# Optimization experiments

Hardware: AMD Instinct MI355X
Metric: run time of the kernel (lower is better)

The kernel has to match this reference:

```python
import jax, jax.numpy as jnp
import numpy as np

B, T, H, V, N_AT, KC, MAX_NB = 512, 64, 512, 780, 40, 4, 8
NMSG = B * T + 1  # message table size; slot 0 = zero padding vector


def setup_inputs() -> dict:
    key = jax.random.key(0)
    ks = jax.random.split(key, 24)
    s = 0.02
    f32 = jnp.float32
    w = lambda k, shp: jax.random.normal(k, shp, f32) * s
    inp = {}
    inp["node_rep"] = jax.random.normal(ks[0], (B, N_AT, H), f32)
    inp["clique_idx"] = jax.random.randint(ks[1], (B, T, KC), 0, N_AT)
    inp["root_clique_idx"] = jax.random.randint(ks[2], (B, KC), 0, N_AT)
    inp["nei_h_idx"] = jax.random.randint(ks[3], (B, T, MAX_NB), 0, NMSG)
    inp["nei_o_idx"] = jax.random.randint(ks[4], (B, T, MAX_NB), 0, NMSG)
    inp["root_nei_idx"] = jax.random.randint(ks[5], (B, MAX_NB), 0, NMSG)
    inp["direction"] = jax.random.randint(ks[6], (B, T), 0, 2)
    inp["pred_target"] = jax.random.randint(ks[7], (B, T), 0, V)
    inp["W_z_w"] = w(ks[8], (2 * H, H)); inp["W_z_b"] = jnp.zeros((H,), f32)
    inp["W_r_w"] = w(ks[9], (H, H));     inp["W_r_b"] = jnp.zeros((H,), f32)
    inp["U_r_w"] = w(ks[10], (H, H))  # no bias in torch U_r
    inp["W_h_w"] = w(ks[11], (2 * H, H)); inp["W_h_b"] = jnp.zeros((H,), f32)
    inp["W_w"] = w(ks[12], (H, H));     inp["W_b"] = jnp.zeros((H,), f32)
    inp["U_w"] = w(ks[13], (2 * H, H)); inp["U_b"] = jnp.zeros((H,), f32)
    inp["W_o_w"] = w(ks[14], (H, V));   inp["W_o_b"] = jnp.zeros((V,), f32)
    inp["U_s_w"] = w(ks[15], (H, 1));   inp["U_s_b"] = jnp.zeros((1,), f32)
    return inp


def _gru(x, h_nei, W_z_w, W_z_b, W_r_w, W_r_b, U_r_w, W_h_w, W_h_b):
    # x: [B,H]; h_nei: [B,MAX_NB,H]  (tree-GRU from the torch GRU() helper)
    sum_h = h_nei.sum(axis=1)
    z = jax.nn.sigmoid(jnp.concatenate([x, sum_h], axis=1) @ W_z_w + W_z_b)
    r = jax.nn.sigmoid((x @ W_r_w + W_r_b)[:, None, :] + h_nei @ U_r_w)
    sum_g = (r * h_nei).sum(axis=1)
    pre_h = jnp.tanh(jnp.concatenate([x, sum_g], axis=1) @ W_h_w + W_h_b)
    return (1.0 - z) * sum_h + z * pre_h


def reference(node_rep, clique_idx, root_clique_idx, nei_h_idx, nei_o_idx,
              root_nei_idx, direction, pred_target,
              W_z_w, W_z_b, W_r_w, W_r_b, U_r_w, W_h_w, W_h_b,
              W_w, W_b, U_w, U_b, W_o_w, W_o_b, U_s_w, U_s_b):
    dt = node_rep.dtype
    b_ar = jnp.arange(B)
    # x features: sum of node_rep over clique atom indices (torch index_select+sum)
    x_all = node_rep[b_ar[:, None, None], clique_idx].sum(axis=2)      # [B,T,H]
    root_x = node_rep[b_ar[:, None], root_clique_idx].sum(axis=1)      # [B,H]
    msg_ids = b_ar[:, None] * T + jnp.arange(T)[None, :] + 1           # [B,T]
    table0 = jnp.zeros((NMSG, H), dt)                                  # h dict -> flat table

    def step(table, xs):
        x_t, h_idx, o_idx, mid = xs
        h_nei = table[h_idx]                      # [B,MAX_NB,H] gather (excl. parent, pre-padded)
        new_h = _gru(x_t, h_nei, W_z_w, W_z_b, W_r_w, W_r_b, U_r_w, W_h_w, W_h_b)
        o = table[o_idx].sum(axis=1)              # [B,H] all-neighbor sum for stop head
        table = table.at[mid].set(new_h)          # scatter message back (h[x,y] = new_h)
        return table, (new_h, o)

    xs = (x_all.transpose(1, 0, 2), nei_h_idx.transpose(1, 0, 2),
          nei_o_idx.transpose(1, 0, 2), msg_ids.T)
    table, (new_h_all, o_all) = jax.lax.scan(step, table0, xs)
    new_h_all = new_h_all.transpose(1, 0, 2).reshape(B * T, H)         # [BT,H]
    o_all = o_all.transpose(1, 0, 2)                                   # [B,T,H]

    # stop head: all steps + final root step (target 0)
    stop_h = jnp.concatenate([x_all, o_all], axis=2).reshape(B * T, 2 * H)
    root_o = table[root_nei_idx].sum(axis=1)
    root_stop = jnp.concatenate([root_x, root_o], axis=1)
    stop_hiddens = jnp.concatenate([stop_h, root_stop], axis=0)        # [BT+B,2H]
    stop_targets = jnp.concatenate([direction.reshape(-1).astype(dt), jnp.zeros((B,), dt)])
    stop_scores = (jax.nn.relu(stop_hiddens @ U_w + U_b) @ U_s_w + U_s_b)[:, 0]
    # BCEWithLogits, sum reduction, / len(mol_batch)
    stop_loss = jnp.sum(jax.nn.softplus(stop_scores) - stop_scores * stop_targets) / B
    stop_acc = jnp.mean(((stop_scores >= 0).astype(dt) == stop_targets).astype(dt))

    # pred head on new_h where direction == 1
    pred_scores = jax.nn.relu(new_h_all @ W_w + W_b) @ W_o_w + W_o_b   # [BT,V]
    logp = jax.nn.log_softmax(pred_scores, axis=-1)
    tgt = pred_target.reshape(-1)
    ce = -jnp.take_along_axis(logp, tgt[:, None], axis=1)[:, 0]
    pmask = (direction.reshape(-1) == 1).astype(dt)
    pred_loss = jnp.sum(ce * pmask) / B                                # CE sum / len(mol_batch)
    preds = jnp.argmax(pred_scores, axis=1)
    pred_acc = jnp.sum((preds == tgt).astype(dt) * pmask) / jnp.sum(pmask)
    return (pred_loss, stop_loss, pred_acc, stop_acc)
```

## Files before the change

### kernel.cpp

```cpp
#include <hip/hip_runtime.h>
#include <math.h>

constexpr int B    = 512;
constexpr int T    = 64;
constexpr int H    = 512;
constexpr int V    = 780;
constexpr int N_AT = 40;
constexpr int KC   = 4;
constexpr int NB   = 8;
constexpr int BT   = B * T;
constexpr int NMSG = BT + 1;

template<int ASRC, int NSEG, int EPI>
__device__ __forceinline__ void gemm_core(
    float* smem, int bx, int by,
    const float* __restrict__ A1, const float* __restrict__ A2, int lda,
    const float* __restrict__ W, const float* __restrict__ bias,
    float* __restrict__ C, int ldc,
    const int* __restrict__ gidx, int gt, const float* __restrict__ table,
    const float* __restrict__ node_rep, const int* __restrict__ cliq,
    const float* __restrict__ o_all,
    const int* __restrict__ rci, const int* __restrict__ rni,
    const float* __restrict__ Ez, const float* __restrict__ Esh,
    const float* __restrict__ Usw, float* __restrict__ partial)
{
    float* As = smem;
    float* Ws = smem + 32 * 68;
    const int tid  = threadIdx.x;
    const int row0 = bx * 64;
    const int col0 = by * 64;
    const int tm   = tid >> 4;
    const int tn   = tid & 15;

    float acc[4][4] = {};

    const int ar0 = tid >> 5;
    const int ac  = tid & 31;
    const int wk0 = tid >> 6;
    const int wc  = tid & 63;

    for (int seg = 0; seg < NSEG; ++seg) {
        const float* Aseg = seg ? A2 : A1;
        const float* Wseg = W + (size_t)seg * H * H;
        for (int k0 = 0; k0 < H; k0 += 32) {
#pragma unroll
            for (int it = 0; it < 8; ++it) {
                const int r    = ar0 + it * 8;
                const int grow = row0 + r;
                float v;
                if (ASRC == 0) {
                    v = Aseg[(size_t)grow * lda + k0 + ac];
                } else if (ASRC == 1) {
                    const int gi = gidx[((grow >> 3) * T + gt) * NB + (grow & 7)];
                    v = table[(size_t)gi * H + k0 + ac];
                } else if (ASRC == 2) {
                    const int* ci = cliq + (size_t)grow * KC;
                    const int  b  = grow >> 6;
                    v = 0.f;
#pragma unroll
                    for (int j = 0; j < KC; ++j)
                        v += node_rep[((size_t)b * N_AT + ci[j]) * H + k0 + ac];
                } else {
                    if (grow < BT) {
                        if (seg == 0) {
                            const int* ci = cliq + (size_t)grow * KC;
                            const int  b  = grow >> 6;
                            v = 0.f;
#pragma unroll
                            for (int j = 0; j < KC; ++j)
                                v += node_rep[((size_t)b * N_AT + ci[j]) * H + k0 + ac];
                        } else {
                            v = o_all[(size_t)grow * H + k0 + ac];
                        }
                    } else {
                        const int b = grow - BT;
                        v = 0.f;
                        if (seg == 0) {
#pragma unroll
                            for (int j = 0; j < KC; ++j)
                                v += node_rep[((size_t)b * N_AT + rci[b * KC + j]) * H + k0 + ac];
                        } else {
#pragma unroll
                            for (int n = 0; n < NB; ++n)
                                v += table[(size_t)rni[b * NB + n] * H + k0 + ac];
                        }
                    }
                }
                As[(size_t)ac * 68 + r] = v;
                const int kk = wk0 + it * 4;
                Ws[(size_t)kk * 68 + wc] = Wseg[(size_t)(k0 + kk) * H + col0 + wc];
            }
            __syncthreads();
#pragma unroll
            for (int kk = 0; kk < 32; ++kk) {
                float a[4], w[4];
                *(float4*)a = *(const float4*)&As[kk * 68 + tm * 4];
                *(float4*)w = *(const float4*)&Ws[kk * 68 + tn * 4];
#pragma unroll
                for (int i = 0; i < 4; ++i)
#pragma unroll
                    for (int j = 0; j < 4; ++j)
                        acc[i][j] = fmaf(a[i], w[j], acc[i][j]);
            }
            __syncthreads();
        }
    }

    if (EPI == 4) {
        float* sred = smem + 2 * 32 * 68;
#pragma unroll
        for (int i = 0; i < 4; ++i) {
            float s = 0.f;
#pragma unroll
            for (int j = 0; j < 4; ++j) {
                const int ccol = col0 + tn * 4 + j;
                float val = acc[i][j] + bias[ccol];
                val = fmaxf(val, 0.f);
                s += val * Usw[ccol];
            }
            sred[(size_t)(tm * 4 + i) * 17 + tn] = s;
        }
        __syncthreads();
        if (tid < 64) {
            float s = 0.f;
#pragma unroll
            for (int t2 = 0; t2 < 16; ++t2) s += sred[(size_t)tid * 17 + t2];
            partial[(size_t)(row0 + tid) * 8 + by] = s;
        }
    } else {
#pragma unroll
        for (int i = 0; i < 4; ++i) {
            const int r = row0 + tm * 4 + i;
            float out[4];
#pragma unroll
            for (int j = 0; j < 4; ++j) {
                const int ccol = col0 + tn * 4 + j;
                float val = acc[i][j] + (bias ? bias[ccol] : 0.f);
                if (EPI == 1) {
                    val = 1.f / (1.f + expf(-val));
                } else if (EPI == 2) {
                    const float ph = tanhf(val);
                    const float zz = Ez[(size_t)r * H + ccol];
                    const float sh = Esh[(size_t)r * H + ccol];
                    val = (1.f - zz) * sh + zz * ph;
                } else if (EPI == 3) {
                    val = fmaxf(val, 0.f);
                }
                out[j] = val;
            }
            *(float4*)&C[(size_t)r * ldc + col0 + tn * 4] = *(float4*)out;
        }
    }
}

constexpr size_t SM_GEMM = (size_t)(2 * 32 * 68) * 4;
constexpr size_t SM_STOP = (size_t)(2 * 32 * 68 + 64 * 17) * 4;

template<int ASRC, int NSEG, int EPI>
__global__ __launch_bounds__(256)
void gemm_g(const float* __restrict__ A1, const float* __restrict__ A2, int lda,
            const float* __restrict__ W, const float* __restrict__ bias,
            float* __restrict__ C, int ldc,
            const int* __restrict__ gidx, int gt, const float* __restrict__ table,
            const float* __restrict__ node_rep, const int* __restrict__ cliq,
            const float* __restrict__ o_all,
            const int* __restrict__ rci, const int* __restrict__ rni,
            const float* __restrict__ Ez, const float* __restrict__ Esh,
            const float* __restrict__ Usw, float* __restrict__ partial)
{
    extern __shared__ float smem[];
    gemm_core<ASRC, NSEG, EPI>(smem, blockIdx.x, blockIdx.y, A1, A2, lda, W, bias,
                               C, ldc, gidx, gt, table, node_rep, cliq, o_all,
                               rci, rni, Ez, Esh, Usw, partial);
}

__global__ __launch_bounds__(256)
void step1_kernel(const int* __restrict__ nei_h, int t, const float* __restrict__ table,
                  const float* __restrict__ Urw, float* __restrict__ hU,
                  const float* __restrict__ xs, const float* __restrict__ Wzw,
                  const float* __restrict__ Wzb, float* __restrict__ zb)
{
    extern __shared__ float smem[];
    if (blockIdx.x < 64) {
        gemm_core<1, 1, 0>(smem, blockIdx.x, blockIdx.y, nullptr, nullptr, 0,
                           Urw, nullptr, hU, H, nei_h, t, table,
                           nullptr, nullptr, nullptr, nullptr, nullptr,
                           nullptr, nullptr, nullptr, nullptr);
    } else {
        gemm_core<0, 2, 1>(smem, blockIdx.x - 64, blockIdx.y, xs, xs + H, 2 * H,
                           Wzw, Wzb, zb, H, nullptr, 0, nullptr,
                           nullptr, nullptr, nullptr, nullptr, nullptr,
                           nullptr, nullptr, nullptr, nullptr);
    }
}

__global__ __launch_bounds__(256)
void pre2_kernel(const float* __restrict__ node_rep, const int* __restrict__ clique_idx,
                 const int* __restrict__ nei_h, const int* __restrict__ nei_o,
                 const float* __restrict__ table,
                 float* __restrict__ xs, float* __restrict__ hs, float* __restrict__ ss,
                 float* __restrict__ sumh, float* __restrict__ oDst, int oStride, int t)
{
    const int i = blockIdx.x * 256 + threadIdx.x;
    const int b = i >> 9, h = i & 511;
    const int* ci = clique_idx + ((size_t)b * T + t) * KC;
    float x = 0.f;
#pragma unroll
    for (int k = 0; k < KC; ++k)
        x += node_rep[((size_t)b * N_AT + ci[k]) * H + h];
    const int* hi = nei_h + ((size_t)b * T + t) * NB;
    const int* oi = nei_o + ((size_t)b * T + t) * NB;
    float sh = 0.f, so = 0.f;
#pragma unroll
    for (int n = 0; n < NB; ++n) {
        sh += table[(size_t)hi[n] * H + h];
        so += table[(size_t)oi[n] * H + h];
    }
    xs[(size_t)b * 1024 + h]       = x;
    xs[(size_t)b * 1024 + 512 + h] = sh;
    hs[(size_t)b * 1024 + h]       = x;
    ss[(size_t)b * 1024 + h]       = x;
    sumh[i] = sh;
    oDst[(size_t)b * oStride + h] = so;
}

__global__ __launch_bounds__(256)
void rsum2_kernel(const float* __restrict__ xrP, int xrStride,
                  const float* __restrict__ hU, const float* __restrict__ table,
                  const int* __restrict__ nei_h, float* __restrict__ hs, int t)
{
    const int i = blockIdx.x * 256 + threadIdx.x;
    const int b = i >> 9, h = i & 511;
    const int* hi = nei_h + ((size_t)b * T + t) * NB;
    const float xrv = xrP[(size_t)b * xrStride + h];
    float s = 0.f;
#pragma unroll
    for (int n = 0; n < NB; ++n) {
        const float hu = hU[((size_t)b * NB + n) * H + h];
        const float r  = 1.f / (1.f + expf(-(xrv + hu)));
        s += r * table[(size_t)hi[n] * H + h];
    }
    hs[(size_t)b * 1024 + 512 + h] = s;
}

__global__ __launch_bounds__(256)
void rootpre_kernel(const float* __restrict__ node_rep, const int* __restrict__ rci,
                    const int* __restrict__ rni, const float* __restrict__ table,
                    float* __restrict__ ss)
{
    const int i = blockIdx.x * 256 + threadIdx.x;
    const int b = i >> 9, h = i & 511;
    float x = 0.f;
#pragma unroll
    for (int k = 0; k < KC; ++k)
        x += node_rep[((size_t)b * N_AT + rci[b * KC + k]) * H + h];
    float so = 0.f;
#pragma unroll
    for (int n = 0; n < NB; ++n)
        so += table[(size_t)rni[b * NB + n] * H + h];
    ss[(size_t)b * 1024 + h]       = x;
    ss[(size_t)b * 1024 + 512 + h] = so;
}

__global__ __launch_bounds__(64)
void stopdot_kernel(const float* __restrict__ s1, const float* __restrict__ Usw,
                    const float* __restrict__ Usb,
                    float* __restrict__ out, int outStride, int outBase)
{
    const int b = blockIdx.x;
    const int lane = threadIdx.x;
    const float* row = s1 + (size_t)b * H;
    float s = 0.f;
    for (int h = lane; h < H; h += 64) s += row[h] * Usw[h];
#pragma unroll
    for (int off = 32; off; off >>= 1) s += __shfl_down(s, off);
    if (lane == 0) out[outBase + b * outStride] = s + Usb[0];
}

__global__ __launch_bounds__(256)
void stoploss_kernel(const float* __restrict__ scores, const int* __restrict__ direction,
                     float* __restrict__ accum)
{
    const int i = blockIdx.x * 256 + threadIdx.x;
    float loss = 0.f, acc = 0.f;
    if (i < BT + B) {
        const float s   = scores[i];
        const float tgt = (i < BT) ? (float)direction[i] : 0.f;
        loss = fmaxf(s, 0.f) - s * tgt + log1pf(expf(-fabsf(s)));
        const float p = (s >= 0.f) ? 1.f : 0.f;
        acc = (p == tgt) ? 1.f : 0.f;
    }
#pragma unroll
    for (int off = 32; off; off >>= 1) {
        loss += __shfl_down(loss, off);
        acc  += __shfl_down(acc, off);
    }
    if ((threadIdx.x & 63) == 0) {
        atomicAdd(&accum[3], loss);
        atomicAdd(&accum[4], acc);
    }
}

__global__ __launch_bounds__(256)
void stopfin_kernel(const float* __restrict__ partial, const float* __restrict__ Usb,
                    const int* __restrict__ direction, float* __restrict__ accum)
{
    const int i = blockIdx.x * 256 + threadIdx.x;
    float loss = 0.f, acc = 0.f;
    {
        float s = Usb[0];
#pragma unroll
        for (int cb = 0; cb < 8; ++cb) s += partial[(size_t)i * 8 + cb];
        const float tgt = (i < BT) ? (float)direction[i] : 0.f;
        loss = fmaxf(s, 0.f) - s * tgt + log1pf(expf(-fabsf(s)));
        const float p = (s >= 0.f) ? 1.f : 0.f;
        acc = (p == tgt) ? 1.f : 0.f;
    }
#pragma unroll
    for (int off = 32; off; off >>= 1) {
        loss += __shfl_down(loss, off);
        acc  += __shfl_down(acc, off);
    }
    if ((threadIdx.x & 63) == 0) {
        atomicAdd(&accum[3], loss);
        atomicAdd(&accum[4], acc);
    }
}

__global__ __launch_bounds__(256)
void ce_kernel(const float* __restrict__ s1_all, const float* __restrict__ Wo,
               const float* __restrict__ Wob, const int* __restrict__ direction,
               const int* __restrict__ ptgt, float* __restrict__ accum)
{
    __shared__ float s1T[512 * 34];
    __shared__ float Ws[32 * 68];
    __shared__ float blk[3];
    const int tid  = threadIdx.x;
    const int row0 = blockIdx.x * 32;

    for (int idx = tid; idx < 32 * 512; idx += 256) {
        const int r = idx >> 9, k = idx & 511;
        s1T[(size_t)k * 34 + r] = s1_all[(size_t)(row0 + r) * H + k];
    }
    if (tid < 3) blk[tid] = 0.f;
    __syncthreads();

    const int tm = tid >> 4, tn = tid & 15;
    const int tgt0 = ptgt[row0 + tm * 2];
    const int tgt1 = ptgt[row0 + tm * 2 + 1];
    float m0 = -1e30f, m1 = -1e30f, ss0 = 0.f, ss1 = 0.f, st0 = 0.f, st1 = 0.f;
    float bv0 = -1e30f, bv1 = -1e30f;
    int   bj0 = 0, bj1 = 0;

    for (int ct = 0; ct < 13; ++ct) {
        const int col0 = ct * 64;
        float acc[2][4] = {};
        for (int k0 = 0; k0 < 512; k0 += 32) {
#pragma unroll
            for (int it = 0; it < 8; ++it) {
                const int idx = tid + it * 256;
                const int kk = idx >> 6, cc = idx & 63;
                const int col = col0 + cc;
                Ws[(size_t)kk * 68 + cc] = (col < V) ? Wo[(size_t)(k0 + kk) * V + col] : 0.f;
            }
            __syncthreads();
#pragma unroll
            for (int kk = 0; kk < 32; ++kk) {
                const float a0 = s1T[(size_t)(k0 + kk) * 34 + tm * 2];
                const float a1 = s1T[(size_t)(k0 + kk) * 34 + tm * 2 + 1];
                float w[4];
                *(float4*)w = *(const float4*)&Ws[kk * 68 + tn * 4];
#pragma unroll
                for (int j = 0; j < 4; ++j) {
                    acc[0][j] = fmaf(a0, w[j], acc[0][j]);
                    acc[1][j] = fmaf(a1, w[j], acc[1][j]);
                }
            }
            __syncthreads();
        }
#pragma unroll
        for (int j = 0; j < 4; ++j) {
            const int col = col0 + tn * 4 + j;
// ... 76 lines not shown
    for (int j = 0; j < 16; ++j) {
        const int c = tx + j * 32;
        float acc = Wb[c];
        for (int k = 0; k < H; ++k) acc += hs[r][k] * Ww[(size_t)k * H + c];
        s1s[r][c] = fmaxf(acc, 0.f);
    }
    __syncthreads();
    const int row = row0 + r;
    const int tgt = ptgt[row];
    float m = -1e30f, ssum = 0.f, stgt = 0.f;
    float bestv = -1e30f; int bestj = 0;
    for (int v = tx; v < V; v += 32) {
        float sc = Wob[v];
        const float* wcol = Wo + v;
        for (int k = 0; k < H; ++k) sc += s1s[r][k] * wcol[(size_t)k * V];
        if (sc > m) { ssum = ssum * expf(m - sc) + 1.f; m = sc; }
        else        { ssum += expf(sc - m); }
        if (sc > bestv) { bestv = sc; bestj = v; }
        if (v == tgt) stgt = sc;
    }
#pragma unroll
    for (int off = 1; off < 32; off <<= 1) {
        const float om = __shfl_xor(m, off);
        const float os = __shfl_xor(ssum, off);
        const float nm = fmaxf(m, om);
        ssum = ssum * expf(m - nm) + os * expf(om - nm);
        m = nm;
        const float obv = __shfl_xor(bestv, off);
        const int   obj = __shfl_xor(bestj, off);
        if (obv > bestv || (obv == bestv && obj < bestj)) { bestv = obv; bestj = obj; }
        stgt += __shfl_xor(stgt, off);
    }
    if (tx == 0) {
        const float ce   = (m + logf(ssum)) - stgt;
        const float mask = (direction[row] == 1) ? 1.f : 0.f;
        const float corr = (bestj == tgt) ? 1.f : 0.f;
        atomicAdd(&accum[0], ce * mask);
        atomicAdd(&accum[1], mask);
        atomicAdd(&accum[2], corr * mask);
    }
}

__global__ void finalize_kernel(const float* __restrict__ accum, float* __restrict__ out)
{
    if (threadIdx.x == 0) {
        out[0] = accum[0] / (float)B;
        out[1] = accum[3] / (float)B;
        out[2] = accum[2] / accum[1];
        out[3] = accum[4] / (float)(BT + B);
    }
}

extern "C" void kernel_launch(void* const* d_in, const int* in_sizes, int n_in,
                              void* d_out, int out_size, void* d_ws, size_t ws_size,
                              hipStream_t stream)
{
    (void)in_sizes; (void)n_in; (void)out_size;

    const float* node_rep        = (const float*)d_in[0];
    const int*   clique_idx      = (const int*)d_in[1];
    const int*   root_clique_idx = (const int*)d_in[2];
    const int*   nei_h_idx       = (const int*)d_in[3];
    const int*   nei_o_idx       = (const int*)d_in[4];
    const int*   root_nei_idx    = (const int*)d_in[5];
    const int*   direction       = (const int*)d_in[6];
    const int*   pred_target     = (const int*)d_in[7];
    const float* W_z_w = (const float*)d_in[8];
    const float* W_z_b = (const float*)d_in[9];
    const float* W_r_w = (const float*)d_in[10];
    const float* W_r_b = (const float*)d_in[11];
    const float* U_r_w = (const float*)d_in[12];
    const float* W_h_w = (const float*)d_in[13];
    const float* W_h_b = (const float*)d_in[14];
    const float* W_w   = (const float*)d_in[15];
    const float* W_b   = (const float*)d_in[16];
    const float* U_w   = (const float*)d_in[17];
    const float* U_b   = (const float*)d_in[18];
    const float* W_o_w = (const float*)d_in[19];
    const float* W_o_b = (const float*)d_in[20];
    const float* U_s_w = (const float*)d_in[21];
    const float* U_s_b = (const float*)d_in[22];

    float* ws = (float*)d_ws;
    size_t off = 0;
    auto alloc = [&](size_t n) { float* p = ws + off; off += n; return p; };

    float* table  = alloc((size_t)NMSG * H);
    float* hU     = alloc((size_t)B * NB * H);
    float* xs     = alloc((size_t)B * 2 * H);
    float* hs     = alloc((size_t)B * 2 * H);
    float* ss     = alloc((size_t)B * 2 * H);
    float* sumh   = alloc((size_t)B * H);
    float* zb     = alloc((size_t)B * H);
    float* xr     = alloc((size_t)B * H);
    float* stop_scores = alloc(BT + B);
    float* accum  = alloc(8);

    const size_t availF = ws_size / sizeof(float);
    float *s1_all = nullptr, *o_all = nullptr, *partial = nullptr, *xr_all = nullptr;
    if (off + (size_t)BT * H <= availF)                 s1_all = alloc((size_t)BT * H);
    if (off + (size_t)BT * H + (size_t)(BT + B) * 8 <= availF) {
        o_all   = alloc((size_t)BT * H);
        partial = alloc((size_t)(BT + B) * 8);
    }
    if (off + (size_t)BT * H <= availF)                 xr_all = alloc((size_t)BT * H);

    hipMemsetAsync(table, 0, (size_t)NMSG * H * sizeof(float), stream);
    hipMemsetAsync(accum, 0, 8 * sizeof(float), stream);

    const int  BH_blocks = (B * H) / 256;
    const dim3 gSmall(8, 8);
    const dim3 gStep(72, 8);

    if (xr_all) {
        gemm_g<2, 1, 0><<<dim3(BT / 64, 8), 256, SM_GEMM, stream>>>(
            nullptr, nullptr, 0, W_r_w, W_r_b, xr_all, H,
            nullptr, 0, nullptr, node_rep, clique_idx,
            nullptr, nullptr, nullptr, nullptr, nullptr, nullptr, nullptr);
    }

    for (int t = 0; t < T; ++t) {
        float* oDst    = o_all ? (o_all + (size_t)t * H) : (ss + H);
        const int oStr = o_all ? (T * H) : (2 * H);
        pre2_kernel<<<BH_blocks, 256, 0, stream>>>(node_rep, clique_idx, nei_h_idx,
                                                   nei_o_idx, table, xs, hs, ss,
                                                   sumh, oDst, oStr, t);
        step1_kernel<<<gStep, 256, SM_GEMM, stream>>>(nei_h_idx, t, table, U_r_w, hU,
                                                      xs, W_z_w, W_z_b, zb);
        if (!xr_all) {
            gemm_g<0, 1, 0><<<gSmall, 256, SM_GEMM, stream>>>(
                xs, nullptr, 2 * H, W_r_w, W_r_b, xr, H,
                nullptr, 0, nullptr, nullptr, nullptr,
                nullptr, nullptr, nullptr, nullptr, nullptr, nullptr, nullptr);
        }
        const float* xrP   = xr_all ? (xr_all + (size_t)t * H) : xr;
        const int    xrStr = xr_all ? (T * H) : H;
        rsum2_kernel<<<BH_blocks, 256, 0, stream>>>(xrP, xrStr, hU, table,
                                                    nei_h_idx, hs, t);
        gemm_g<0, 2, 2><<<gSmall, 256, SM_GEMM, stream>>>(
            hs, hs + H, 2 * H, W_h_w, W_h_b, table + (size_t)(t + 1) * H, T * H,
            nullptr, 0, nullptr, nullptr, nullptr,
            nullptr, nullptr, nullptr, zb, sumh, nullptr, nullptr);
        if (!o_all) {
            gemm_g<0, 2, 3><<<gSmall, 256, SM_GEMM, stream>>>(
                ss, ss + H, 2 * H, U_w, U_b, zb, H,
                nullptr, 0, nullptr, nullptr, nullptr,
                nullptr, nullptr, nullptr, nullptr, nullptr, nullptr, nullptr);
            stopdot_kernel<<<B, 64, 0, stream>>>(zb, U_s_w, U_s_b, stop_scores, T, t);
        }
    }

    if (o_all) {
        gemm_g<3, 2, 4><<<dim3((BT + B) / 64, 8), 256, SM_STOP, stream>>>(
            nullptr, nullptr, 0, U_w, U_b, nullptr, 0,
            nullptr, 0, table, node_rep, clique_idx,
            o_all, root_clique_idx, root_nei_idx, nullptr, nullptr, U_s_w, partial);
        stopfin_kernel<<<(BT + B) / 256, 256, 0, stream>>>(partial, U_s_b, direction, accum);
    } else {
        rootpre_kernel<<<BH_blocks, 256, 0, stream>>>(node_rep, root_clique_idx,
                                                      root_nei_idx, table, ss);
        gemm_g<0, 2, 3><<<gSmall, 256, SM_GEMM, stream>>>(
            ss, ss + H, 2 * H, U_w, U_b, zb, H,
            nullptr, 0, nullptr, nullptr, nullptr,
            nullptr, nullptr, nullptr, nullptr, nullptr, nullptr, nullptr);
        stopdot_kernel<<<B, 64, 0, stream>>>(zb, U_s_w, U_s_b, stop_scores, 1, BT);
        stoploss_kernel<<<(BT + B + 255) / 256, 256, 0, stream>>>(stop_scores, direction, accum);
    }

    if (s1_all) {
        gemm_g<0, 1, 3><<<dim3(BT / 64, 8), 256, SM_GEMM, stream>>>(
            table + H, nullptr, H, W_w, W_b, s1_all, H,
            nullptr, 0, nullptr, nullptr, nullptr,
            nullptr, nullptr, nullptr, nullptr, nullptr, nullptr, nullptr);
        ce_kernel<<<BT / 32, 256, 0, stream>>>(s1_all, W_o_w, W_o_b,
                                               direction, pred_target, accum);
    } else {
        predhead_kernel<<<BT / PH_ROWS, 256, 0, stream>>>(table, W_w, W_b, W_o_w, W_o_b,
                                                          direction, pred_target, accum);
    }

    finalize_kernel<<<1, 64, 0, stream>>>(accum, (float*)d_out);
}
```

Before: 13.48 ms.

## Replace per-step kernel launches with persistent cooperative GRU loop kernel

Rewrites the sequential tree-GRU time loop as a single cooperative kernel. It uses grid-wide syncs between three phases per step (z/h GEMM with x prefetch, U_r/W_r GEMMs, gated neighbour sums), which replaces roughly six kernel launches per step. It also precomputes U_r projections per message row in a table-sized buffer, masks neighbours that are not yet valid by timestep index, and fuses the z and h GEMMs into one tile pass. It keeps a multi-launch fallback if the cooperative launch fails. The risk is grid.sync overhead and using only 256 blocks of small 32x64 tiles, which leaves less parallelism per phase.

```diff
diff --git a/kernel.cpp b/kernel.cpp
--- a/kernel.cpp
+++ b/kernel.cpp
@@ -1,5 +1,8 @@
 #include <hip/hip_runtime.h>
+#include <hip/hip_cooperative_groups.h>
 #include <math.h>
+
+namespace cg = cooperative_groups;
 
 constexpr int B    = 512;
 constexpr int T    = 64;
@@ -10,67 +13,386 @@
 constexpr int NB   = 8;
 constexpr int BT   = B * T;
 constexpr int NMSG = BT + 1;
+constexpr int BH   = B * H;
+
+__device__ __forceinline__ float sigf(float x) { return 1.f / (1.f + expf(-x)); }
+
+
+__device__ __forceinline__ void ph_zh(int t, int bx, int tid,
+    float* As1, float* As2, float* W1s, float* W2s,
+    const float* __restrict__ xb, const float* __restrict__ sumh,
+    const float* __restrict__ sumg,
+    const float* __restrict__ Wz, const float* __restrict__ bz,
+    const float* __restrict__ Wh, const float* __restrict__ bh,
+    float* __restrict__ table)
+{
+    const int rt = bx >> 3, ct = bx & 7, row0 = rt * 32, col0 = ct * 64;
+    const int tm = tid >> 4, tn = tid & 15;
+    const int ak = tid & 31, am0 = tid >> 5, wn = tid & 63, wk0 = tid >> 6;
+    float az[2][4] = {}, ah[2][4] = {};
+
+    for (int k0 = 0; k0 < H; k0 += 32) {
+#pragma unroll
+        for (int it = 0; it < 4; ++it) {
+            const int m = am0 + it * 8;
+            As1[ak * 38 + m] = xb[(size_t)(row0 + m) * H + k0 + ak];
+        }
+#pragma unroll
+        for (int it = 0; it < 8; ++it) {
+            const int kk = wk0 + it * 4;
+            W1s[kk * 68 + wn] = Wz[(size_t)(k0 + kk) * H + col0 + wn];
+            W2s[kk * 68 + wn] = Wh[(size_t)(k0 + kk) * H + col0 + wn];
+        }
+        __syncthreads();
+#pragma unroll
+        for (int kk = 0; kk < 32; ++kk) {
+            const float a0 = As1[kk * 38 + tm * 2];
+            const float a1 = As1[kk * 38 + tm * 2 + 1];
+            float w1[4], w2[4];
+            *(float4*)w1 = *(const float4*)&W1s[kk * 68 + tn * 4];
+            *(float4*)w2 = *(const float4*)&W2s[kk * 68 + tn * 4];
+#pragma unroll
+            for (int j = 0; j < 4; ++j) {
+                az[0][j] = fmaf(a0, w1[j], az[0][j]);
+                az[1][j] = fmaf(a1, w1[j], az[1][j]);
+                ah[0][j] = fmaf(a0, w2[j], ah[0][j]);
+                ah[1][j] = fmaf(a1, w2[j], ah[1][j]);
+            }
+        }
+        __syncthreads();
+    }
+    for (int k0 = 0; k0 < H; k0 += 32) {
+#pragma unroll
+        for (int it = 0; it < 4; ++it) {
+            const int m = am0 + it * 8;
+            As1[ak * 38 + m] = sumh[(size_t)(row0 + m) * H + k0 + ak];
+            As2[ak * 38 + m] = sumg[(size_t)(row0 + m) * H + k0 + ak];
+        }
+#pragma unroll
+        for (int it = 0; it < 8; ++it) {
+            const int kk = wk0 + it * 4;
+            W1s[kk * 68 + wn] = Wz[(size_t)(H + k0 + kk) * H + col0 + wn];
+            W2s[kk * 68 + wn] = Wh[(size_t)(H + k0 + kk) * H + col0 + wn];
+        }
+        __syncthreads();
+#pragma unroll
+        for (int kk = 0; kk < 32; ++kk) {
+            const float a10 = As1[kk * 38 + tm * 2];
+            const float a11 = As1[kk * 38 + tm * 2 + 1];
+            const float a20 = As2[kk * 38 + tm * 2];
+            const float a21 = As2[kk * 38 + tm * 2 + 1];
+            float w1[4], w2[4];
+            *(float4*)w1 = *(const float4*)&W1s[kk * 68 + tn * 4];
+            *(float4*)w2 = *(const float4*)&W2s[kk * 68 + tn * 4];
+#pragma unroll
+            for (int j = 0; j < 4; ++j) {
+                az[0][j] = fmaf(a10, w1[j], az[0][j]);
+                az[1][j] = fmaf(a11, w1[j], az[1][j]);
+                ah[0][j] = fmaf(a20, w2[j], ah[0][j]);
+                ah[1][j] = fmaf(a21, w2[j], ah[1][j]);
+            }
+        }
+        __syncthreads();
+    }
+#pragma unroll
+    for (int i = 0; i < 2; ++i) {
+        const int b = row0 + tm * 2 + i;
+        const float4 s4 = *(const float4*)&sumh[(size_t)b * H + col0 + tn * 4];
+        const float sv[4] = {s4.x, s4.y, s4.z, s4.w};
+        float out[4];
+#pragma unroll
+        for (int j = 0; j < 4; ++j) {
+            const int c = col0 + tn * 4 + j;
+            const float z  = sigf(az[i][j] + bz[c]);
+            const float ph = tanhf(ah[i][j] + bh[c]);
+            out[j] = (1.f - z) * sv[j] + z * ph;
+        }
+        *(float4*)&table[((size_t)b * T + t + 1) * H + col0 + tn * 4] = *(float4*)out;
+    }
+}
+
+template<int AS>
+__device__ __forceinline__ void tile_g(int bx, int tid, float* As, float* Ws_,
+    const float* __restrict__ Abase, int tpos,
+    const int* __restrict__ nh, int tstep,
+    const float* __restrict__ W, const float* __restrict__ bias,
+    float* __restrict__ C)
+{
+    const int rt = bx >> 3, ct = bx & 7, row0 = rt * 32, col0 = ct * 64;
+    const int tm = tid >> 4, tn = tid & 15;
+    const int ak = tid & 31, am0 = tid >> 5, wn = tid & 63, wk0 = tid >> 6;
+    float ac[2][4] = {};
+
+    for (int k0 = 0; k0 < H; k0 += 32) {
+#pragma unroll
+        for (int it = 0; it < 4; ++it) {
+            const int m = am0 + it * 8, gm = row0 + m;
+            float v;
+            if (AS == 0) {
+                v = Abase[(size_t)gm * H + k0 + ak];
+            } else if (AS == 1) {
+                v = Abase[((size_t)gm * T + tpos) * H + k0 + ak];
+            } else {
+                const int b = gm >> 3, n = gm & 7;
+                const int gi = nh[((size_t)b * T + tstep) * NB + n];
+                v = (gi != 0 && ((gi - 1) & 63) == tstep)
+                        ? 0.f : Abase[(size_t)gi * H + k0 + ak];
+            }
+            As[ak * 38 + m] = v;
+        }
+#pragma unroll
+        for (int it = 0; it < 8; ++it) {
+            const int kk = wk0 + it * 4;
+            Ws_[kk * 68 + wn] = W[(size_t)(k0 + kk) * H + col0 + wn];
+        }
+        __syncthreads();
+#pragma unroll
+        for (int kk = 0; kk < 32; ++kk) {
+            const float a0 = As[kk * 38 + tm * 2];
+            const float a1 = As[kk * 38 + tm * 2 + 1];
+            float w[4];
+            *(float4*)w = *(const float4*)&Ws_[kk * 68 + tn * 4];
+#pragma unroll
+            for (int j = 0; j < 4; ++j) {
+                ac[0][j] = fmaf(a0, w[j], ac[0][j]);
+                ac[1][j] = fmaf(a1, w[j], ac[1][j]);
+            }
+        }
+        __syncthreads();
+    }
+#pragma unroll
+    for (int i = 0; i < 2; ++i) {
+        const int gm = row0 + tm * 2 + i;
+        float out[4];
+#pragma unroll
+        for (int j = 0; j < 4; ++j)
+            out[j] = ac[i][j] + (bias ? bias[col0 + tn * 4 + j] : 0.f);
+        float* dst = (AS == 1) ? &C[((size_t)gm * T + tpos) * H + col0 + tn * 4]
+                               : &C[(size_t)gm * H + col0 + tn * 4];
+        *(float4*)dst = *(float4*)out;
+    }
+}
+
+__device__ __forceinline__ void ph_xgather(int tg, int unit,
+    const float* __restrict__ node_rep, const int* __restrict__ cliq,
+    float* __restrict__ xb)
+{
+    const int b = unit >> 7, h4 = (unit & 127) * 4;
+    const int* ci = cliq + ((size_t)b * T + tg) * KC;
+    float4 s = {0.f, 0.f, 0.f, 0.f};
+#pragma unroll
+    for (int j = 0; j < KC; ++j) {
+        const float4 v = *(const float4*)&node_rep[((size_t)b * N_AT + ci[j]) * H + h4];
+        s.x += v.x; s.y += v.y; s.z += v.z; s.w += v.w;
+    }
+    *(float4*)&xb[(size_t)b * H + h4] = s;
+}
+
+template<bool USETU>
+__device__ __forceinline__ void ph_sums(int tg, int unit,
+    const int* __restrict__ nh, const float* __restrict__ xr,
+    const float* __restrict__ table, const float* __restrict__ tu,
+    const float* __restrict__ hU,
+    float* __restrict__ sumh, float* __restrict__ sumg)
+{
+    const int b = unit >> 7, h4 = (unit & 127) * 4;
+    const int* hi = nh + ((size_t)b * T + tg) * NB;
+    const float4 x4 = *(const float4*)&xr[(size_t)b * H + h4];
+    float4 sh = {0.f, 0.f, 0.f, 0.f}, sg = {0.f, 0.f, 0.f, 0.f};
+#pragma unroll
+    for (int n = 0; n < NB; ++n) {
+        const int idx = hi[n];
+        float4 hv = {0.f, 0.f, 0.f, 0.f};
+        if (!(idx != 0 && ((idx - 1) & 63) == tg))
+            hv = *(const float4*)&table[(size_t)idx * H + h4];
+        const float4 hu = USETU ? *(const float4*)&tu[(size_t)idx * H + h4]
+                                : *(const float4*)&hU[((size_t)b * NB + n) * H + h4];
+        sh.x += hv.x; sh.y += hv.y; sh.z += hv.z; sh.w += hv.w;
+        sg.x += hv.x * sigf(x4.x + hu.x);
+        sg.y += hv.y * sigf(x4.y + hu.y);
+        sg.z += hv.z * sigf(x4.z + hu.z);
+        sg.w += hv.w * sigf(x4.w + hu.w);
+    }
+    *(float4*)&sumh[(size_t)b * H + h4] = sh;
+    *(float4*)&sumg[(size_t)b * H + h4] = sg;
+}
+
+template<bool USETU>
+__global__ __launch_bounds__(256)
+void loop_k(const int* __restrict__ nei_h, const float* __restrict__ node_rep,
+            const int* __restrict__ cliq,
+            const float* __restrict__ Wz, const float* __restrict__ bz,
+            const float* __restrict__ Wh, const float* __restrict__ bh,
+            const float* __restrict__ Ur, const float* __restrict__ Wr,
+            const float* __restrict__ br,
+            float* table, float* tu, float* hU,
+            float* xb0, float* xb1, float* xrb, float* sumh, float* sumg)
+{
+    cg::grid_group grid = cg::this_grid();
+    __shared__ float As1[32 * 38], As2[32 * 38], W1s[32 * 68], W2s[32 * 68];
+    const int bid = blockIdx.x, tid = threadIdx.x;
+
+    for (int t = 0; t < T; ++t) {
+        float* xbc = (t & 1) ? xb1 : xb0;
+        float* xbn = (t & 1) ? xb0 : xb1;
+        if (bid < 128) {
+            ph_zh(t, bid, tid, As1, As2, W1s, W2s, xbc, sumh, sumg,
+                  Wz, bz, Wh, bh, table);
+        } else if (t + 1 < T) {
+            const int base = (bid - 128) * 512 + tid;
+            ph_xgather(t + 1, base,       node_rep, cliq, xbn);
+            ph_xgather(t + 1, base + 256, node_rep, cliq, xbn);
+        }
+        if (t + 1 == T) break;
+        grid.sync();
+        if (USETU) {
+            if (bid < 128)
+                tile_g<1>(bid, tid, As1, W1s, table, t + 1, nullptr, 0,
+                          Ur, nullptr, tu);
+            else
+                tile_g<0>(bid - 128, tid, As1, W1s, xbn, 0, nullptr, 0,
+                          Wr, br, xrb);
+        } else {
+#pragma unroll
+            for (int q = 0; q < 4; ++q)
+                tile_g<2>(bid * 4 + q, tid, As1, W1s, table, 0, nei_h, t + 1,
+                          Ur, nullptr, hU);
+            if (bid < 128)
+                tile_g<0>(bid, tid, As1, W1s, xbn, 0, nullptr, 0, Wr, br, xrb);
+        }
+        grid.sync();
+        ph_sums<USETU>(t + 1, bid * 256 + tid, nei_h, xrb, table, tu, hU,
+                       sumh, sumg);
+        grid.sync();
+    }
+}
+
+__global__ __launch_bounds__(256)
+void kA_k(int t, const float* xbc, float* xbn, const float* sumh, const float* sumg,
+          const float* Wz, const float* bz, const float* Wh, const float* bh,
+          float* table, const float* node_rep, const int* cliq)
+{
+    __shared__ float As1[32 * 38], As2[32 * 38], W1s[32 * 68], W2s[32 * 68];
+    if (blockIdx.x < 128) {
+        ph_zh(t, blockIdx.x, threadIdx.x, As1, As2, W1s, W2s, xbc, sumh, sumg,
+              Wz, bz, Wh, bh, table);
+    } else if (t + 1 < T) {
+        const int base = (blockIdx.x - 128) * 512 + threadIdx.x;
+        ph_xgather(t + 1, base,       node_rep, cliq, xbn);
+        ph_xgather(t + 1, base + 256, node_rep, cliq, xbn);
+    }
+}
+template<bool USETU>
+__global__ __launch_bounds__(256)
+void kB_k(int t, const float* table, float* tu, float* hU, const float* xbn,
+          const float* Ur, const float* Wr, const float* br, float* xrb,
+          const int* nei_h)
+{
+    __shared__ float As1[32 * 38], W1s[32 * 68];
+    if (USETU) {
+        if (blockIdx.x < 128)
+            tile_g<1>(blockIdx.x, threadIdx.x, As1, W1s, table, t + 1,
+                      nullptr, 0, Ur, nullptr, tu);
+        else
+            tile_g<0>(blockIdx.x - 128, threadIdx.x, As1, W1s, xbn, 0,
+                      nullptr, 0, Wr, br, xrb);
+    } else {
+#pragma unroll
+        for (int q = 0; q < 4; ++q)
+            tile_g<2>(blockIdx.x * 4 + q, threadIdx.x, As1, W1s, table, 0,
+                      nei_h, t + 1, Ur, nullptr, hU);
+        if (blockIdx.x < 128)
+            tile_g<0>(blockIdx.x, threadIdx.x, As1, W1s, xbn, 0, nullptr, 0,
+                      Wr, br, xrb);
+    }
+}
+template<bool USETU>
+__global__ __launch_bounds__(256)
+void kC_k(int t, const int* nei_h, const float* xrb, const float* table,
+          const float* tu, const float* hU, float* sumh, float* sumg)
+{
+    ph_sums<USETU>(t + 1, blockIdx.x * 256 + threadIdx.x, nei_h, xrb, table,
+                   tu, hU, sumh, sumg);
+}
+
+__global__ __launch_bounds__(256)
+void xg0_k(const float* __restrict__ node_rep, const int* __restrict__ cliq,
+           float* __restrict__ xb)
+{
+    ph_xgather(0, blockIdx.x * 256 + threadIdx.x, node_rep, cliq, xb);
+}
+
+__global__ __launch_bounds__(256)
+void oall_k(const int* __restrict__ nei_o, const float* __restrict__ table,
+            float* __restrict__ o_all)
+{
+    const int i = blockIdx.x * 256 + threadIdx.x;
+    const int m = i >> 7, h4 = (i & 127) * 4;
+    const int t = m & 63;
+    const int* oi = nei_o + (size_t)m * NB;
+    float4 s = {0.f, 0.f, 0.f, 0.f};
+#pragma unroll
+    for (int n = 0; n < NB; ++n) {
+        const int idx = oi[n];
+        if (idx != 0 && ((idx - 1) & 63) < t) {
+            const float4 hv = *(const float4*)&table[(size_t)idx * H + h4];
+            s.x += hv.x; s.y += hv.y; s.z += hv.z; s.w += hv.w;
+        }
+    }
+    *(float4*)&o_all[(size_t)m * H + h4] = s;
+}
+
+constexpr size_t SM_GEMM = (size_t)(2 * 32 * 68) * 4;
+constexpr size_t SM_STOP = (size_t)(2 * 32 * 68 + 64 * 17) * 4;
 
 template<int ASRC, int NSEG, int EPI>
-__device__ __forceinline__ void gemm_core(
-    float* smem, int bx, int by,
-    const float* __restrict__ A1, const float* __restrict__ A2, int lda,
-    const float* __restrict__ W, const float* __restrict__ bias,
-    float* __restrict__ C, int ldc,
-    const int* __restrict__ gidx, int gt, const float* __restrict__ table,
-    const float* __restrict__ node_rep, const int* __restrict__ cliq,
-    const float* __restrict__ o_all,
-    const int* __restrict__ rci, const int* __restrict__ rni,
-    const float* __restrict__ Ez, const float* __restrict__ Esh,
-    const float* __restrict__ Usw, float* __restrict__ partial)
-{
+__global__ __launch_bounds__(256)
+void gemm_g(const float* __restrict__ A1, const float* __restrict__ A2, int lda,
+            const float* __restrict__ W, const float* __restrict__ bias,
+            float* __restrict__ C, int ldc,
+            const float* __restrict__ node_rep, const int* __restrict__ cliq,
+            const int* __restrict__ rci, const int* __restrict__ rni,
+            const int* __restrict__ neio, const float* __restrict__ table,
+            const float* __restrict__ Usw, float* __restrict__ partial)
+{
+    extern __shared__ float smem[];
     float* As = smem;
     float* Ws = smem + 32 * 68;
-    const int tid  = threadIdx.x;
-    const int row0 = bx * 64;
-    const int col0 = by * 64;
-    const int tm   = tid >> 4;
-    const int tn   = tid & 15;
-
+    const int tid = threadIdx.x, row0 = blockIdx.x * 64, col0 = blockIdx.y * 64;
+    const int tm = tid >> 4, tn = tid & 15;
+    const int ar0 = tid >> 5, ac = tid & 31, wk0 = tid >> 6, wc = tid & 63;
     float acc[4][4] = {};
 
-    const int ar0 = tid >> 5;
-    const int ac  = tid & 31;
-    const int wk0 = tid >> 6;
-    const int wc  = tid & 63;
-
     for (int seg = 0; seg < NSEG; ++seg) {
-        const float* Aseg = seg ? A2 : A1;
         const float* Wseg = W + (size_t)seg * H * H;
         for (int k0 = 0; k0 < H; k0 += 32) {
 #pragma unroll
             for (int it = 0; it < 8; ++it) {
-                const int r    = ar0 + it * 8;
-                const int grow = row0 + r;
+                const int r = ar0 + it * 8, grow = row0 + r;
                 float v;
                 if (ASRC == 0) {
-                    v = Aseg[(size_t)grow * lda + k0 + ac];
-                } else if (ASRC == 1) {
-                    const int gi = gidx[((grow >> 3) * T + gt) * NB + (grow & 7)];
-                    v = table[(size_t)gi * H + k0 + ac];
-                } else if (ASRC == 2) {
-                    const int* ci = cliq + (size_t)grow * KC;
-                    const int  b  = grow >> 6;
-                    v = 0.f;
-#pragma unroll
-                    for (int j = 0; j < KC; ++j)
-                        v += node_rep[((size_t)b * N_AT + ci[j]) * H + k0 + ac];
+                    v = A1[(size_t)grow * lda + k0 + ac];
                 } else {
                     if (grow < BT) {
                         if (seg == 0) {
                             const int* ci = cliq + (size_t)grow * KC;
-                            const int  b  = grow >> 6;
+                            const int b = grow >> 6;
                             v = 0.f;
 #pragma unroll
                             for (int j = 0; j < KC; ++j)
                                 v += node_rep[((size_t)b * N_AT + ci[j]) * H + k0 + ac];
+                        } else if (ASRC == 3) {
+                            v = A2[(size_t)grow * H + k0 + ac];
                         } else {
-                            v = o_all[(size_t)grow * H + k0 + ac];
+                            const int tt = grow & 63;
+                            const int* oi = neio + (size_t)grow * NB;
+                            v = 0.f;
+#pragma unroll
+                            for (int n = 0; n < NB; ++n) {
+                                const int idx = oi[n];
+                                if (idx != 0 && ((idx - 1) & 63) < tt)
+                                    v += table[(size_t)idx * H + k0 + ac];
+                            }
                         }
                     } else {
                         const int b = grow - BT;
@@ -113,10 +435,8 @@
             float s = 0.f;
 #pragma unroll
             for (int j = 0; j < 4; ++j) {
-                const int ccol = col0 + tn * 4 + j;
-                float val = acc[i][j] + bias[ccol];
-                val = fmaxf(val, 0.f);
-                s += val * Usw[ccol];
+                const int c = col0 + tn * 4 + j;
+                s += fmaxf(acc[i][j] + bias[c], 0.f) * Usw[c];
             }
             sred[(size_t)(tm * 4 + i) * 17 + tn] = s;
         }
@@ -124,8 +444,8 @@
         if (tid < 64) {
             float s = 0.f;
 #pragma unroll
-            for (int t2 = 0; t2 < 16; ++t2) s += sred[(size_t)tid * 17 + t2];
-            partial[(size_t)(row0 + tid) * 8 + by] = s;
+            for (int q = 0; q < 16; ++q) s += sred[(size_t)tid * 17 + q];
+            partial[(size_t)(row0 + tid) * 8 + blockIdx.y] = s;
         }
     } else {
 #pragma unroll
@@ -134,170 +454,12 @@
             float out[4];
 #pragma unroll
             for (int j = 0; j < 4; ++j) {
-                const int ccol = col0 + tn * 4 + j;
-                float val = acc[i][j] + (bias ? bias[ccol] : 0.f);
-                if (EPI == 1) {
-                    val = 1.f / (1.f + expf(-val));
-                } else if (EPI == 2) {
-                    const float ph = tanhf(val);
-                    const float zz = Ez[(size_t)r * H + ccol];
-                    const float sh = Esh[(size_t)r * H + ccol];
-                    val = (1.f - zz) * sh + zz * ph;
-                } else if (EPI == 3) {
-                    val = fmaxf(val, 0.f);
-                }
+                float val = acc[i][j] + (bias ? bias[col0 + tn * 4 + j] : 0.f);
+                if (EPI == 3) val = fmaxf(val, 0.f);
                 out[j] = val;
             }
             *(float4*)&C[(size_t)r * ldc + col0 + tn * 4] = *(float4*)out;
         }
-    }
-}
-
-constexpr size_t SM_GEMM = (size_t)(2 * 32 * 68) * 4;
-constexpr size_t SM_STOP = (size_t)(2 * 32 * 68 + 64 * 17) * 4;
-
-template<int ASRC, int NSEG, int EPI>
-__global__ __launch_bounds__(256)
-void gemm_g(const float* __restrict__ A1, const float* __restrict__ A2, int lda,
-            const float* __restrict__ W, const float* __restrict__ bias,
-            float* __restrict__ C, int ldc,
-            const int* __restrict__ gidx, int gt, const float* __restrict__ table,
-            const float* __restrict__ node_rep, const int* __restrict__ cliq,
-            const float* __restrict__ o_all,
-            const int* __restrict__ rci, const int* __restrict__ rni,
-            const float* __restrict__ Ez, const float* __restrict__ Esh,
-            const float* __restrict__ Usw, float* __restrict__ partial)
-{
-    extern __shared__ float smem[];
-    gemm_core<ASRC, NSEG, EPI>(smem, blockIdx.x, blockIdx.y, A1, A2, lda, W, bias,
-                               C, ldc, gidx, gt, table, node_rep, cliq, o_all,
-                               rci, rni, Ez, Esh, Usw, partial);
-}
-
-__global__ __launch_bounds__(256)
-void step1_kernel(const int* __restrict__ nei_h, int t, const float* __restrict__ table,
-                  const float* __restrict__ Urw, float* __restrict__ hU,
-                  const float* __restrict__ xs, const float* __restrict__ Wzw,
-                  const float* __restrict__ Wzb, float* __restrict__ zb)
-{
-    extern __shared__ float smem[];
-    if (blockIdx.x < 64) {
-        gemm_core<1, 1, 0>(smem, blockIdx.x, blockIdx.y, nullptr, nullptr, 0,
-                           Urw, nullptr, hU, H, nei_h, t, table,
-                           nullptr, nullptr, nullptr, nullptr, nullptr,
-                           nullptr, nullptr, nullptr, nullptr);
-    } else {
-        gemm_core<0, 2, 1>(smem, blockIdx.x - 64, blockIdx.y, xs, xs + H, 2 * H,
-                           Wzw, Wzb, zb, H, nullptr, 0, nullptr,
-                           nullptr, nullptr, nullptr, nullptr, nullptr,
-                           nullptr, nullptr, nullptr, nullptr);
-    }
-}
-
-__global__ __launch_bounds__(256)
-void pre2_kernel(const float* __restrict__ node_rep, const int* __restrict__ clique_idx,
-                 const int* __restrict__ nei_h, const int* __restrict__ nei_o,
-                 const float* __restrict__ table,
-                 float* __restrict__ xs, float* __restrict__ hs, float* __restrict__ ss,
-                 float* __restrict__ sumh, float* __restrict__ oDst, int oStride, int t)
-{
-    const int i = blockIdx.x * 256 + threadIdx.x;
-    const int b = i >> 9, h = i & 511;
-    const int* ci = clique_idx + ((size_t)b * T + t) * KC;
-    float x = 0.f;
-#pragma unroll
-    for (int k = 0; k < KC; ++k)
-        x += node_rep[((size_t)b * N_AT + ci[k]) * H + h];
-    const int* hi = nei_h + ((size_t)b * T + t) * NB;
-    const int* oi = nei_o + ((size_t)b * T + t) * NB;
-    float sh = 0.f, so = 0.f;
-#pragma unroll
-    for (int n = 0; n < NB; ++n) {
-        sh += table[(size_t)hi[n] * H + h];
-        so += table[(size_t)oi[n] * H + h];
-    }
-    xs[(size_t)b * 1024 + h]       = x;
-    xs[(size_t)b * 1024 + 512 + h] = sh;
-    hs[(size_t)b * 1024 + h]       = x;
-    ss[(size_t)b * 1024 + h]       = x;
-    sumh[i] = sh;
-    oDst[(size_t)b * oStride + h] = so;
-}
-
-__global__ __launch_bounds__(256)
-void rsum2_kernel(const float* __restrict__ xrP, int xrStride,
-                  const float* __restrict__ hU, const float* __restrict__ table,
-                  const int* __restrict__ nei_h, float* __restrict__ hs, int t)
-{
-    const int i = blockIdx.x * 256 + threadIdx.x;
-    const int b = i >> 9, h = i & 511;
-    const int* hi = nei_h + ((size_t)b * T + t) * NB;
-    const float xrv = xrP[(size_t)b * xrStride + h];
-    float s = 0.f;
-#pragma unroll
-    for (int n = 0; n < NB; ++n) {
-        const float hu = hU[((size_t)b * NB + n) * H + h];
-        const float r  = 1.f / (1.f + expf(-(xrv + hu)));
-        s += r * table[(size_t)hi[n] * H + h];
-    }
-    hs[(size_t)b * 1024 + 512 + h] = s;
-}
-
-__global__ __launch_bounds__(256)
-void rootpre_kernel(const float* __restrict__ node_rep, const int* __restrict__ rci,
-                    const int* __restrict__ rni, const float* __restrict__ table,
-                    float* __restrict__ ss)
-{
-    const int i = blockIdx.x * 256 + threadIdx.x;
-    const int b = i >> 9, h = i & 511;
-    float x = 0.f;
-#pragma unroll
-    for (int k = 0; k < KC; ++k)
-        x += node_rep[((size_t)b * N_AT + rci[b * KC + k]) * H + h];
-    float so = 0.f;
-#pragma unroll
-    for (int n = 0; n < NB; ++n)
-        so += table[(size_t)rni[b * NB + n] * H + h];
-    ss[(size_t)b * 1024 + h]       = x;
-    ss[(size_t)b * 1024 + 512 + h] = so;
-}
-
-__global__ __launch_bounds__(64)
-void stopdot_kernel(const float* __restrict__ s1, const float* __restrict__ Usw,
-                    const float* __restrict__ Usb,
-                    float* __restrict__ out, int outStride, int outBase)
-{
-    const int b = blockIdx.x;
-    const int lane = threadIdx.x;
-    const float* row = s1 + (size_t)b * H;
-    float s = 0.f;
-    for (int h = lane; h < H; h += 64) s += row[h] * Usw[h];
-#pragma unroll
-    for (int off = 32; off; off >>= 1) s += __shfl_down(s, off);
-    if (lane == 0) out[outBase + b * outStride] = s + Usb[0];
-}
-
-__global__ __launch_bounds__(256)
-void stoploss_kernel(const float* __restrict__ scores, const int* __restrict__ direction,
-                     float* __restrict__ accum)
-{
-    const int i = blockIdx.x * 256 + threadIdx.x;
-    float loss = 0.f, acc = 0.f;
-    if (i < BT + B) {
-        const float s   = scores[i];
-        const float tgt = (i < BT) ? (float)direction[i] : 0.f;
-        loss = fmaxf(s, 0.f) - s * tgt + log1pf(expf(-fabsf(s)));
-        const float p = (s >= 0.f) ? 1.f : 0.f;
-        acc = (p == tgt) ? 1.f : 0.f;
-    }
-#pragma unroll
-    for (int off = 32; off; off >>= 1) {
-        loss += __shfl_down(loss, off);
-        acc  += __shfl_down(acc, off);
-    }
-    if ((threadIdx.x & 63) == 0) {
-        atomicAdd(&accum[3], loss);
-        atomicAdd(&accum[4], acc);
     }
 }
 
@@ -540,100 +702,102 @@
     const float* U_s_b = (const float*)d_in[22];
 
     float* ws = (float*)d_ws;
+    const size_t availF = ws_size / sizeof(float);
     size_t off = 0;
     auto alloc = [&](size_t n) { float* p = ws + off; off += n; return p; };
 
-    float* table  = alloc((size_t)NMSG * H);
-    float* hU     = alloc((size_t)B * NB * H);
-    float* xs     = alloc((size_t)B * 2 * H);
-    float* hs     = alloc((size_t)B * 2 * H);
-    float* ss     = alloc((size_t)B * 2 * H);
-    float* sumh   = alloc((size_t)B * H);
-    float* zb     = alloc((size_t)B * H);
-    float* xr     = alloc((size_t)B * H);
-    float* stop_scores = alloc(BT + B);
-    float* accum  = alloc(8);
-
-    const size_t availF = ws_size / sizeof(float);
-    float *s1_all = nullptr, *o_all = nullptr, *partial = nullptr, *xr_all = nullptr;
-    if (off + (size_t)BT * H <= availF)                 s1_all = alloc((size_t)BT * H);
-    if (off + (size_t)BT * H + (size_t)(BT + B) * 8 <= availF) {
-        o_all   = alloc((size_t)BT * H);
-        partial = alloc((size_t)(BT + B) * 8);
-    }
-    if (off + (size_t)BT * H <= availF)                 xr_all = alloc((size_t)BT * H);
+    float* table   = alloc((size_t)NMSG * H);
+    float* xb0     = alloc(BH);
+    float* xb1     = alloc(BH);
+    float* xrb     = alloc(BH);
+    float* sumh    = alloc(BH);
+    float* sumg    = alloc(BH);
+    float* partial = alloc((size_t)(BT + B) * 8);
+    float* accum   = alloc(8);
+
+    float* tu = nullptr;
+    float* hU = nullptr;
+    if (off + (size_t)NMSG * H <= availF) tu = alloc((size_t)NMSG * H);
+    else                                  hU = alloc((size_t)B * NB * H);
 
     hipMemsetAsync(table, 0, (size_t)NMSG * H * sizeof(float), stream);
+    if (tu) hipMemsetAsync(tu, 0, (size_t)NMSG * H * sizeof(float), stream);
+    hipMemsetAsync(sumh, 0, (size_t)BH * sizeof(float), stream);
+    hipMemsetAsync(sumg, 0, (size_t)BH * sizeof(float), stream);
     hipMemsetAsync(accum, 0, 8 * sizeof(float), stream);
 
-    const int  BH_blocks = (B * H) / 256;
-    const dim3 gSmall(8, 8);
-    const dim3 gStep(72, 8);
-
-    if (xr_all) {
-        gemm_g<2, 1, 0><<<dim3(BT / 64, 8), 256, SM_GEMM, stream>>>(
-            nullptr, nullptr, 0, W_r_w, W_r_b, xr_all, H,
-            nullptr, 0, nullptr, node_rep, clique_idx,
-            nullptr, nullptr, nullptr, nullptr, nullptr, nullptr, nullptr);
-    }
-
-    for (int t = 0; t < T; ++t) {
-        float* oDst    = o_all ? (o_all + (size_t)t * H) : (ss + H);
-        const int oStr = o_all ? (T * H) : (2 * H);
-        pre2_kernel<<<BH_blocks, 256, 0, stream>>>(node_rep, clique_idx, nei_h_idx,
-                                                   nei_o_idx, table, xs, hs, ss,
-                                                   sumh, oDst, oStr, t);
-        step1_kernel<<<gStep, 256, SM_GEMM, stream>>>(nei_h_idx, t, table, U_r_w, hU,
-                                                      xs, W_z_w, W_z_b, zb);
-        if (!xr_all) {
-            gemm_g<0, 1, 0><<<gSmall, 256, SM_GEMM, stream>>>(
-                xs, nullptr, 2 * H, W_r_w, W_r_b, xr, H,
-                nullptr, 0, nullptr, nullptr, nullptr,
-                nullptr, nullptr, nullptr, nullptr, nullptr, nullptr, nullptr);
-        }
-        const float* xrP   = xr_all ? (xr_all + (size_t)t * H) : xr;
-        const int    xrStr = xr_all ? (T * H) : H;
-        rsum2_kernel<<<BH_blocks, 256, 0, stream>>>(xrP, xrStr, hU, table,
-                                                    nei_h_idx, hs, t);
-        gemm_g<0, 2, 2><<<gSmall, 256, SM_GEMM, stream>>>(
-            hs, hs + H, 2 * H, W_h_w, W_h_b, table + (size_t)(t + 1) * H, T * H,
-            nullptr, 0, nullptr, nullptr, nullptr,
-            nullptr, nullptr, nullptr, zb, sumh, nullptr, nullptr);
-        if (!o_all) {
-            gemm_g<0, 2, 3><<<gSmall, 256, SM_GEMM, stream>>>(
-                ss, ss + H, 2 * H, U_w, U_b, zb, H,
-                nullptr, 0, nullptr, nullptr, nullptr,
-                nullptr, nullptr, nullptr, nullptr, nullptr, nullptr, nullptr);
-            stopdot_kernel<<<B, 64, 0, stream>>>(zb, U_s_w, U_s_b, stop_scores, T, t);
-        }
-    }
-
-    if (o_all) {
+    xg0_k<<<256, 256, 0, stream>>>(node_rep, clique_idx, xb0);
+
+    {
+        const int*   a0  = nei_h_idx;
+        const float* a1  = node_rep;
+        const int*   a2  = clique_idx;
+        const float* a3  = W_z_w; const float* a4 = W_z_b;
+        const float* a5  = W_h_w; const float* a6 = W_h_b;
+        const float* a7  = U_r_w; const float* a8 = W_r_w; const float* a9 = W_r_b;
+        float* a10 = table; float* a11 = tu; float* a12 = hU;
+        float* a13 = xb0; float* a14 = xb1; float* a15 = xrb;
+        float* a16 = sumh; float* a17 = sumg;
+        void* kargs[] = {(void*)&a0, (void*)&a1, (void*)&a2, (void*)&a3,
+                         (void*)&a4, (void*)&a5, (void*)&a6, (void*)&a7,
+                         (void*)&a8, (void*)&a9, (void*)&a10, (void*)&a11,
+                         (void*)&a12, (void*)&a13, (void*)&a14, (void*)&a15,
+                         (void*)&a16, (void*)&a17};
+        hipError_t err;
+        if (tu)
+            err = hipLaunchCooperativeKernel(loop_k<true>, dim3(256), dim3(256),
+                                             kargs, 0, stream);
+        else
+            err = hipLaunchCooperativeKernel(loop_k<false>, dim3(256), dim3(256),
+                                             kargs, 0, stream);
+        if (err != hipSuccess) {
+            for (int t = 0; t < T; ++t) {
+                float* xbc = (t & 1) ? xb1 : xb0;
+                float* xbn = (t & 1) ? xb0 : xb1;
+                kA_k<<<256, 256, 0, stream>>>(t, xbc, xbn, sumh, sumg,
+                                              W_z_w, W_z_b, W_h_w, W_h_b,
+                                              table, node_rep, clique_idx);
+                if (t + 1 == T) break;
+                if (tu) {
+                    kB_k<true><<<256, 256, 0, stream>>>(t, table, tu, hU, xbn,
+                                                        U_r_w, W_r_w, W_r_b, xrb,
+                                                        nei_h_idx);
+                    kC_k<true><<<256, 256, 0, stream>>>(t, nei_h_idx, xrb, table,
+                                                        tu, hU, sumh, sumg);
+                } else {
+                    kB_k<false><<<256, 256, 0, stream>>>(t, table, tu, hU, xbn,
+                                                         U_r_w, W_r_w, W_r_b, xrb,
+                                                         nei_h_idx);
+                    kC_k<false><<<256, 256, 0, stream>>>(t, nei_h_idx, xrb, table,
+                                                         tu, hU, sumh, sumg);
+                }
+            }
+        }
+    }
+
+    if (tu) {
+        oall_k<<<BT * H / 4 / 256, 256, 0, stream>>>(nei_o_idx, table, tu);
         gemm_g<3, 2, 4><<<dim3((BT + B) / 64, 8), 256, SM_STOP, stream>>>(
+            nullptr, tu, 0, U_w, U_b, nullptr, 0,
+            node_rep, clique_idx, root_clique_idx, root_nei_idx,
+            nullptr, table, U_s_w, partial);
+    } else {
+        gemm_g<7, 2, 4><<<dim3((BT + B) / 64, 8), 256, SM_STOP, stream>>>(
             nullptr, nullptr, 0, U_w, U_b, nullptr, 0,
-            nullptr, 0, table, node_rep, clique_idx,
-            o_all, root_clique_idx, root_nei_idx, nullptr, nullptr, U_s_w, partial);
-        stopfin_kernel<<<(BT + B) / 256, 256, 0, stream>>>(partial, U_s_b, direction, accum);
-    } else {
-        rootpre_kernel<<<BH_blocks, 256, 0, stream>>>(node_rep, root_clique_idx,
-                                                      root_nei_idx, table, ss);
-        gemm_g<0, 2, 3><<<gSmall, 256, SM_GEMM, stream>>>(
-            ss, ss + H, 2 * H, U_w, U_b, zb, H,
-            nullptr, 0, nullptr, nullptr, nullptr,
-            nullptr, nullptr, nullptr, nullptr, nullptr, nullptr, nullptr);
-        stopdot_kernel<<<B, 64, 0, stream>>>(zb, U_s_w, U_s_b, stop_scores, 1, BT);
-        stoploss_kernel<<<(BT + B + 255) / 256, 256, 0, stream>>>(stop_scores, direction, accum);
-    }
-
-    if (s1_all) {
+            node_rep, clique_idx, root_clique_idx, root_nei_idx,
+            nei_o_idx, table, U_s_w, partial);
+    }
+    stopfin_kernel<<<(BT + B) / 256, 256, 0, stream>>>(partial, U_s_b, direction, accum);
+
+    if (tu) {
         gemm_g<0, 1, 3><<<dim3(BT / 64, 8), 256, SM_GEMM, stream>>>(
-            table + H, nullptr, H, W_w, W_b, s1_all, H,
-            nullptr, 0, nullptr, nullptr, nullptr,
-            nullptr, nullptr, nullptr, nullptr, nullptr, nullptr, nullptr);
-        ce_kernel<<<BT / 32, 256, 0, stream>>>(s1_all, W_o_w, W_o_b,
+            table + H, nullptr, H, W_w, W_b, tu, H,
+            nullptr, nullptr, nullptr, nullptr, nullptr, nullptr, nullptr, nullptr);
+        ce_kernel<<<BT / 32, 256, 0, stream>>>(tu, W_o_w, W_o_b,
                                                direction, pred_target, accum);
     } else {
-        predhead_kernel<<<BT / PH_ROWS, 256, 0, stream>>>(table, W_w, W_b, W_o_w, W_o_b,
+        predhead_kernel<<<BT / PH_ROWS, 256, 0, stream>>>(table, W_w, W_b,
+                                                          W_o_w, W_o_b,
                                                           direction, pred_target, accum);
     }
 
```

Result: slower. 24.66 ms (+82.9%).
